# Performance work log

Measured on AMD Instinct MI355X. Metric: run time of the kernel, lower is better.

## Reference

```python
import jax, jax.numpy as jnp
import numpy as np

N_NODES = 50000
DEG = 16
N_EDGES = N_NODES * DEG
IN_FEATS = 256
NUM_HEADS = 4
OUT_FEATS = 64
NEG_SLOPE = 0.2


def setup_inputs() -> dict:
    key = jax.random.key(0)
    k1, k2, k3, k4, k5, k6 = jax.random.split(key, 6)
    row_ptr = jnp.arange(N_NODES + 1, dtype=jnp.int64 if jax.config.jax_enable_x64 else jnp.int32) * DEG
    col_ind = jax.random.randint(k1, (N_EDGES,), 0, N_NODES)
    # CSC mirrors (used only by the fused op's backward pass; math-inert here)
    col_ptr = jnp.arange(N_NODES + 1, dtype=row_ptr.dtype) * DEG
    row_ind = jax.random.randint(k2, (N_EDGES,), 0, N_NODES)
    feat = jax.random.normal(k3, (N_NODES, IN_FEATS), dtype=jnp.float32)
    # Glorot-style init for params
    g = float(np.sqrt(2.0))  # gain for relu
    std_W = g * np.sqrt(2.0 / (IN_FEATS + OUT_FEATS * NUM_HEADS))
    W = jax.random.normal(k4, (IN_FEATS, OUT_FEATS * NUM_HEADS), dtype=jnp.float32) * std_W
    std_a = g * np.sqrt(2.0 / (1 + NUM_HEADS * OUT_FEATS))
    attn_l = jax.random.normal(k5, (1, NUM_HEADS, OUT_FEATS), dtype=jnp.float32) * std_a
    attn_r = jax.random.normal(k6, (1, NUM_HEADS, OUT_FEATS), dtype=jnp.float32) * std_a
    return {"row_ptr": row_ptr, "col_ind": col_ind, "col_ptr": col_ptr,
            "row_ind": row_ind, "feat": feat, "W": W, "attn_l": attn_l, "attn_r": attn_r}


def reference(row_ptr, col_ind, col_ptr, row_ind, feat, W, attn_l, attn_r):
    N = feat.shape[0]
    E = col_ind.shape[0]
    # Dense projection: [N, H, F]
    h = jnp.matmul(feat, W).reshape(N, NUM_HEADS, OUT_FEATS)
    attn_row = jnp.sum(attn_l * h, axis=-1)  # [N, H] (dst scores)
    attn_col = jnp.sum(attn_r * h, axis=-1)  # [N, H] (src scores)
    # Recover destination node id per edge from CSR row_ptr
    dst = jnp.searchsorted(row_ptr, jnp.arange(E), side="right") - 1  # [E]
    src = col_ind  # [E]
    # Edge score: LeakyReLU(attn_row[dst] + attn_col[src])
    e = attn_row[dst] + attn_col[src]  # [E, H]
    e = jnp.where(e > 0, e, NEG_SLOPE * e)
    # Segment softmax over each destination's neighborhood
    e_max = jax.ops.segment_max(e, dst, num_segments=N)  # [N, H]
    ex = jnp.exp(e - e_max[dst])  # [E, H]
    denom = jax.ops.segment_sum(ex, dst, num_segments=N)  # [N, H]
    alpha = ex / denom[dst]  # [E, H]
    # Weighted scatter-add aggregation of source features
    out = jax.ops.segment_sum(h[src] * alpha[:, :, None], dst, num_segments=N)  # [N, H, F]
    return out
```

## Files before the change

### kernel.cpp

```cpp
#include <hip/hip_runtime.h>
#include <hip/hip_bf16.h>

#define DEG        16
#define IN_FEATS   256
#define NUM_HEADS  4
#define OUT_FEATS  64
#define HF         256
#define NEG_SLOPE  0.2f

#define CPITCH 264

typedef __attribute__((ext_vector_type(8))) short  short8;
typedef __attribute__((ext_vector_type(4))) float  floatx4;
typedef unsigned short ushortT;

__device__ __forceinline__ unsigned short f2bf(float f) {
    union { float f; unsigned u; } v; v.f = f;
    unsigned r = v.u + 0x7fffu + ((v.u >> 16) & 1u);
    return (unsigned short)(r >> 16);
}
__device__ __forceinline__ float bf2f(unsigned short u) {
    union { unsigned u; float f; } v; v.u = ((unsigned)u) << 16;
    return v.f;
}
__device__ __forceinline__ unsigned pk2(float lo, float hi) {
    return (unsigned)f2bf(lo) | ((unsigned)f2bf(hi) << 16);
}

__device__ __forceinline__ void load16_g2l(const void* g, void* lds) {
    __builtin_amdgcn_global_load_lds(
        (const __attribute__((address_space(1))) unsigned int*)(unsigned long long)g,
        (__attribute__((address_space(3))) unsigned int*)(unsigned int)(unsigned long long)lds,
        16, 0, 0);
}

__global__ __launch_bounds__(256) void prep(
    const float* __restrict__ feat, const float* __restrict__ W,
    ushortT* __restrict__ featb, ushortT* __restrict__ Wt,
    int nfb, long long totalElems)
{
    int b = blockIdx.x;
    if (b < nfb) {
        long long base = (long long)b * 2048 + (long long)threadIdx.x * 8;
        if (base + 8 <= totalElems) {
            float4 v0 = *(const float4*)&feat[base];
            float4 v1 = *(const float4*)&feat[base + 4];
            uint4 o;
            o.x = pk2(v0.x, v0.y); o.y = pk2(v0.z, v0.w);
            o.z = pk2(v1.x, v1.y); o.w = pk2(v1.z, v1.w);
            *(uint4*)&featb[base] = o;
        }
    } else {
        int n = b - nfb;
        int k = threadIdx.x;
        Wt[n * 256 + k] = f2bf(W[k * 256 + n]);
    }
}

__global__ __launch_bounds__(256, 3) void gat_gemm_mfma2(
    const ushortT* __restrict__ featb,
    const ushortT* __restrict__ Bt,
    const float* __restrict__ attn_l,
    const float* __restrict__ attn_r,
    ushortT* __restrict__ Hb,
    float* __restrict__ arow,
    float* __restrict__ acol,
    int M)
{
    __shared__ __align__(16) ushortT SMEM[64 * CPITCH];
    ushortT* As = SMEM;
    ushortT* Cs = SMEM;

    const int tid  = threadIdx.x;
    const int wave = tid >> 6;
    const int lane = tid & 63;
    const int l15  = lane & 15;
    const int quad = lane >> 4;
    const int rowBase = blockIdx.x * 64;

    #pragma unroll
    for (int t = 0; t < 8; ++t) {
        int row  = wave * 16 + t * 2 + (lane >> 5);
        int cst  = lane & 31;
        int cg   = cst ^ (row & 7);
        int grow = rowBase + row; if (grow > M - 1) grow = M - 1;
        const ushortT* g = featb + (long long)grow * 256 + cg * 8;
        load16_g2l(g, &As[(wave * 512 + t * 64) * 8]);
    }

    short8 bbuf[2][4];
    #pragma unroll
    for (int ni = 0; ni < 4; ++ni)
        bbuf[0][ni] = *(const short8*)&Bt[(wave * 64 + ni * 16 + l15) * 256 + quad * 8];

    __syncthreads();

    floatx4 acc[4][4] = {};

    #pragma unroll
    for (int ks = 0; ks < 8; ++ks) {
        if (ks < 7) {
            #pragma unroll
            for (int ni = 0; ni < 4; ++ni)
                bbuf[(ks + 1) & 1][ni] = *(const short8*)
                    &Bt[(wave * 64 + ni * 16 + l15) * 256 + (ks + 1) * 32 + quad * 8];
        }
        short8 af[4];
        #pragma unroll
        for (int mi = 0; mi < 4; ++mi) {
            int row = mi * 16 + l15;
            int q   = ks * 4 + quad;
            int cst = q ^ (row & 7);
            af[mi] = *(const short8*)&As[row * 256 + cst * 8];
        }
        #pragma unroll
        for (int mi = 0; mi < 4; ++mi)
            #pragma unroll
            for (int ni = 0; ni < 4; ++ni)
                acc[mi][ni] = __builtin_amdgcn_mfma_f32_16x16x32_bf16(
                    af[mi], bbuf[ks & 1][ni], acc[mi][ni], 0, 0, 0);
    }

    float al[4], ar[4];
    #pragma unroll
    for (int ni = 0; ni < 4; ++ni) {
        al[ni] = attn_l[wave * 64 + ni * 16 + l15];
        ar[ni] = attn_r[wave * 64 + ni * 16 + l15];
    }
    #pragma unroll
    for (int mi = 0; mi < 4; ++mi) {
        #pragma unroll
        for (int reg = 0; reg < 4; ++reg) {
            float pl = 0.f, pr = 0.f;
            #pragma unroll
            for (int ni = 0; ni < 4; ++ni) {
                pl = fmaf(acc[mi][ni][reg], al[ni], pl);
                pr = fmaf(acc[mi][ni][reg], ar[ni], pr);
            }
            #pragma unroll
            for (int off = 8; off >= 1; off >>= 1) {
                pl += __shfl_xor(pl, off, 64);
                pr += __shfl_xor(pr, off, 64);
            }
            if (l15 == 0) {
                int gr = rowBase + mi * 16 + quad * 4 + reg;
                if (gr < M) {
                    arow[gr * NUM_HEADS + wave] = pl;
                    acol[gr * NUM_HEADS + wave] = pr;
                }
            }
        }
    }

    __syncthreads();

    #pragma unroll
    for (int mi = 0; mi < 4; ++mi)
        #pragma unroll
        for (int ni = 0; ni < 4; ++ni)
            #pragma unroll
            for (int reg = 0; reg < 4; ++reg)
                Cs[(mi * 16 + quad * 4 + reg) * CPITCH + wave * 64 + ni * 16 + l15] =
                    f2bf(acc[mi][ni][reg]);
    __syncthreads();

    #pragma unroll
    for (int i = 0; i < 8; ++i) {
        int f  = tid + 256 * i;
        int r  = f >> 5;
        int c8 = (f & 31) << 3;
        int gr = rowBase + r;
        if (gr < M) {
            uint4 v = *(const uint4*)&Cs[r * CPITCH + c8];
            *(uint4*)&Hb[(size_t)gr * HF + c8] = v;
        }
    }
}

__global__ __launch_bounds__(256) void gat_aggregate3(
    const ushortT* __restrict__ Hb,
    const float* __restrict__ arow,
    const float* __restrict__ acol,
    const int* __restrict__ col_ind,
    float* __restrict__ out,
    int N)
{
    const int tid  = threadIdx.x;
    const int wave = tid >> 6;
    const int lane = tid & 63;
    const int n    = blockIdx.x * 4 + wave;
    if (n >= N) return;

    const int j16  = lane & 15;
    const int hd16 = lane >> 4;

    int   src_e = col_ind[n * DEG + j16];
    float e = arow[n * NUM_HEADS + hd16] + acol[src_e * NUM_HEADS + hd16];
    e = (e > 0.f) ? e : NEG_SLOPE * e;

    float m = e;
    #pragma unroll
    for (int off = 8; off >= 1; off >>= 1)
        m = fmaxf(m, __shfl_xor(m, off, 16));
    float ex = __expf(e - m);
    float s = ex;
    #pragma unroll
    for (int off = 8; off >= 1; off >>= 1)
        s += __shfl_xor(s, off, 16);
    float alpha = ex / s;

    const int myHeadBase = (lane >> 4) << 4;
    float acc0 = 0.f, acc1 = 0.f, acc2 = 0.f, acc3 = 0.f;

    #pragma unroll
    for (int j = 0; j < DEG; ++j) {
        int   sj = __shfl(src_e, j, 64);
        float a  = __shfl(alpha, myHeadBase + j, 64);
        uint2 v = *(const uint2*)&Hb[(size_t)sj * HF + lane * 4];
        acc0 = fmaf(a, bf2f((unsigned short)(v.x & 0xffffu)), acc0);
        acc1 = fmaf(a, bf2f((unsigned short)(v.x >> 16)),     acc1);
        acc2 = fmaf(a, bf2f((unsigned short)(v.y & 0xffffu)), acc2);
        acc3 = fmaf(a, bf2f((unsigned short)(v.y >> 16)),     acc3);
    }

    *(float4*)&out[(size_t)n * HF + lane * 4] = make_float4(acc0, acc1, acc2, acc3);
}

extern "C" void kernel_launch(void* const* d_in, const int* in_sizes, int n_in,
                              void* d_out, int out_size, void* d_ws, size_t ws_size,
                              hipStream_t stream) {
    const int*   col_ind = (const int*)  d_in[1];
    const float* feat    = (const float*)d_in[4];
    const float* W       = (const float*)d_in[5];
    const float* attn_l  = (const float*)d_in[6];
    const float* attn_r  = (const float*)d_in[7];
    float* out = (float*)d_out;

    const int N = in_sizes[0] - 1;

    ushortT* featb = (ushortT*)d_out;
    ushortT* Hb    = (ushortT*)d_ws;
    float*   arow  = (float*)(Hb + (size_t)N * HF);
    float*   acol  = arow + (size_t)N * NUM_HEADS;
    ushortT* Wt    = (ushortT*)(acol + (size_t)N * NUM_HEADS);

    const long long totalElems = (long long)N * HF;
    const int nfb = (int)((totalElems + 2047) / 2048);

    prep<<<nfb + 256, 256, 0, stream>>>(feat, W, featb, Wt, nfb, totalElems);

    dim3 ggrid((N + 63) / 64);
    gat_gemm_mfma2<<<ggrid, 256, 0, stream>>>(featb, Wt, attn_l, attn_r,
                                              Hb, arow, acol, N);

    gat_aggregate3<<<(N + 3) / 4, 256, 0, stream>>>(Hb, arow, acol, col_ind, out, N);
}
```

Measured before the change: 198.6 us.

## Store projected features in 8 column slices and aggregate per slice

```diff
diff --git a/kernel.cpp b/kernel.cpp
--- a/kernel.cpp
+++ b/kernel.cpp
@@ -62,7 +62,7 @@
     const ushortT* __restrict__ Bt,
     const float* __restrict__ attn_l,
     const float* __restrict__ attn_r,
-    ushortT* __restrict__ Hb,
+    ushortT* __restrict__ Hs,
     float* __restrict__ arow,
     float* __restrict__ acol,
     int M)
@@ -164,38 +164,40 @@
                     f2bf(acc[mi][ni][reg]);
     __syncthreads();
 
-    #pragma unroll
-    for (int i = 0; i < 8; ++i) {
-        int f  = tid + 256 * i;
-        int r  = f >> 5;
-        int c8 = (f & 31) << 3;
-        int gr = rowBase + r;
-        if (gr < M) {
-            uint4 v = *(const uint4*)&Cs[r * CPITCH + c8];
-            *(uint4*)&Hb[(size_t)gr * HF + c8] = v;
-        }
-    }
-}
-
-__global__ __launch_bounds__(256) void gat_aggregate3(
-    const ushortT* __restrict__ Hb,
+    const size_t strideS = (size_t)M * 32;
+    const int r  = tid >> 2;
+    const int c  = (tid & 3) << 3;
+    const int gr = rowBase + r;
+    if (gr < M) {
+        #pragma unroll
+        for (int s = 0; s < 8; ++s) {
+            uint4 v = *(const uint4*)&Cs[r * CPITCH + s * 32 + c];
+            *(uint4*)&Hs[(size_t)s * strideS + (size_t)gr * 32 + c] = v;
+        }
+    }
+}
+
+__global__ __launch_bounds__(256) void gat_aggregate4(
+    const ushortT* __restrict__ Hs,
     const float* __restrict__ arow,
     const float* __restrict__ acol,
     const int* __restrict__ col_ind,
     float* __restrict__ out,
     int N)
 {
-    const int tid  = threadIdx.x;
-    const int wave = tid >> 6;
-    const int lane = tid & 63;
-    const int n    = blockIdx.x * 4 + wave;
+    const int s    = blockIdx.x & 7;
+    const int head = s >> 1;
+    const int half = s & 1;
+    const int wave = threadIdx.x >> 6;
+    const int lane = threadIdx.x & 63;
+    const int l15  = lane & 15;
+    const int n    = (blockIdx.x >> 3) * 4 + wave;
     if (n >= N) return;
 
-    const int j16  = lane & 15;
-    const int hd16 = lane >> 4;
-
-    int   src_e = col_ind[n * DEG + j16];
-    float e = arow[n * NUM_HEADS + hd16] + acol[src_e * NUM_HEADS + hd16];
+    const ushortT* Hslice = Hs + (size_t)s * N * 32;
+
+    int   src_e = col_ind[n * DEG + l15];
+    float e = arow[n * NUM_HEADS + head] + acol[src_e * NUM_HEADS + head];
     e = (e > 0.f) ? e : NEG_SLOPE * e;
 
     float m = e;
@@ -203,27 +205,29 @@
     for (int off = 8; off >= 1; off >>= 1)
         m = fmaxf(m, __shfl_xor(m, off, 16));
     float ex = __expf(e - m);
-    float s = ex;
+    float su = ex;
     #pragma unroll
     for (int off = 8; off >= 1; off >>= 1)
-        s += __shfl_xor(s, off, 16);
-    float alpha = ex / s;
-
-    const int myHeadBase = (lane >> 4) << 4;
-    float acc0 = 0.f, acc1 = 0.f, acc2 = 0.f, acc3 = 0.f;
-
-    #pragma unroll
-    for (int j = 0; j < DEG; ++j) {
+        su += __shfl_xor(su, off, 16);
+    float alpha = ex / su;
+
+    float acc0 = 0.f, acc1 = 0.f;
+    #pragma unroll
+    for (int it = 0; it < 4; ++it) {
+        int   j  = it * 4 + (lane >> 4);
         int   sj = __shfl(src_e, j, 64);
-        float a  = __shfl(alpha, myHeadBase + j, 64);
-        uint2 v = *(const uint2*)&Hb[(size_t)sj * HF + lane * 4];
-        acc0 = fmaf(a, bf2f((unsigned short)(v.x & 0xffffu)), acc0);
-        acc1 = fmaf(a, bf2f((unsigned short)(v.x >> 16)),     acc1);
-        acc2 = fmaf(a, bf2f((unsigned short)(v.y & 0xffffu)), acc2);
-        acc3 = fmaf(a, bf2f((unsigned short)(v.y >> 16)),     acc3);
-    }
-
-    *(float4*)&out[(size_t)n * HF + lane * 4] = make_float4(acc0, acc1, acc2, acc3);
+        float a  = __shfl(alpha, j, 64);
+        unsigned v = *(const unsigned*)&Hslice[(size_t)sj * 32 + l15 * 2];
+        acc0 = fmaf(a, bf2f((unsigned short)(v & 0xffffu)), acc0);
+        acc1 = fmaf(a, bf2f((unsigned short)(v >> 16)),     acc1);
+    }
+    acc0 += __shfl_xor(acc0, 16, 64); acc0 += __shfl_xor(acc0, 32, 64);
+    acc1 += __shfl_xor(acc1, 16, 64); acc1 += __shfl_xor(acc1, 32, 64);
+
+    if (lane < 16) {
+        *(float2*)&out[(size_t)n * HF + head * 64 + half * 32 + l15 * 2] =
+            make_float2(acc0, acc1);
+    }
 }
 
 extern "C" void kernel_launch(void* const* d_in, const int* in_sizes, int n_in,
@@ -239,8 +243,8 @@
     const int N = in_sizes[0] - 1;
 
     ushortT* featb = (ushortT*)d_out;
-    ushortT* Hb    = (ushortT*)d_ws;
-    float*   arow  = (float*)(Hb + (size_t)N * HF);
+    ushortT* Hs    = (ushortT*)d_ws;
+    float*   arow  = (float*)(Hs + (size_t)N * HF);
     float*   acol  = arow + (size_t)N * NUM_HEADS;
     ushortT* Wt    = (ushortT*)(acol + (size_t)N * NUM_HEADS);
 
@@ -251,7 +255,8 @@
 
     dim3 ggrid((N + 63) / 64);
     gat_gemm_mfma2<<<ggrid, 256, 0, stream>>>(featb, Wt, attn_l, attn_r,
-                                              Hb, arow, acol, N);
-
-    gat_aggregate3<<<(N + 3) / 4, 256, 0, stream>>>(Hb, arow, acol, col_ind, out, N);
-}
+                                              Hs, arow, acol, N);
+
+    dim3 agrid(((N + 3) / 4) * 8);
+    gat_aggregate4<<<agrid, 256, 0, stream>>>(Hs, arow, acol, col_ind, out, N);
+}
```

Measured after the change: 232.8 us. 17.2% more time.
